# Kernel optimization log

Measured on AMD Instinct MI355X. Metric: run time of the kernel, lower is better.

Reference implementation:

```python
import jax, jax.numpy as jnp
from jax import lax
import numpy as np

B, N, J, NI, D = 2, 2048, 24, 9, 3
CD, HID = 16, 128
SOFT_BLEND = 20.0
MAX_STEPS, CVG = 50, 1e-5
INIT_BONES = np.array([0, 1, 2, 4, 5, 16, 17, 18, 19])


def _mlp(params, x):
    h = x
    for W, b in params[:-1]:
        h = jax.nn.softplus(h @ W + b)
    W, b = params[-1]
    return h @ W + b


def _broyden(g, x0, J_inv0):
    # x0: [P,3,1], J_inv0: [P,3,3]; fixed MAX_STEPS iterations, track best iterate
    gx = g(x0)
    err0 = jnp.linalg.norm(gx, axis=(1, 2))
    state = (x0, gx, J_inv0, -(J_inv0 @ gx), x0, err0)

    def body(i, st):
        x, gx, Jinv, upd, bx, berr = st
        dx = upd
        x = x + dx
        gx_new = g(x)
        dgx = gx_new - gx
        vT = jnp.swapaxes(dx, -2, -1) @ Jinv            # [P,1,3]
        a = dx - Jinv @ dgx                              # [P,3,1]
        b = vT @ dgx + 1e-6                              # [P,1,1]
        Jinv = Jinv + (a / b) @ vT                       # rank-1 Broyden update
        upd = -(Jinv @ gx_new)
        err = jnp.linalg.norm(gx_new, axis=(1, 2))
        better = err < berr
        bx = jnp.where(better[:, None, None], x, bx)
        berr = jnp.where(better, err, berr)
        return (x, gx_new, Jinv, upd, bx, berr)

    st = lax.fori_loop(0, MAX_STEPS, body, state)
    return st[4], st[5] < CVG


def setup_inputs():
    key = jax.random.key(0)
    ks = jax.random.split(key, 24)
    xd = 0.5 * jax.random.normal(ks[0], (B, N, D), jnp.float32)
    cond_latent = jax.random.normal(ks[1], (B, CD), jnp.float32)
    # near-identity invertible bone transforms
    R = jnp.eye(3, dtype=jnp.float32) + 0.1 * jax.random.normal(ks[2], (B, J, 3, 3), jnp.float32)
    t = 0.1 * jax.random.normal(ks[3], (B, J, 3), jnp.float32)
    tfs = jnp.zeros((B, J, 4, 4), jnp.float32)
    tfs = tfs.at[..., :3, :3].set(R).at[..., :3, 3].set(t).at[..., 3, 3].set(1.0)

    def w(k, fi, fo):
        return jax.random.normal(k, (fi, fo), jnp.float32) / np.sqrt(fi)

    din = D + CD
    inp = dict(xd=xd, cond_latent=cond_latent, tfs=tfs)
    dims_lbs = [(din, HID), (HID, HID), (HID, HID), (HID, J)]
    dims_disp = [(din, HID), (HID, HID), (HID, HID), (HID, D)]
    for i, (fi, fo) in enumerate(dims_lbs):
        inp[f"lbs_w{i}"] = w(ks[4 + i], fi, fo)
        inp[f"lbs_b{i}"] = jnp.zeros((fo,), jnp.float32)
    for i, (fi, fo) in enumerate(dims_disp):
        inp[f"disp_w{i}"] = w(ks[10 + i], fi, fo)
        inp[f"disp_b{i}"] = jnp.zeros((fo,), jnp.float32)
    return inp


def _forward(xd, cond_latent, tfs, lbs, disp):
    P = B * N
    xd_f = xd.reshape(P, D)
    cond_f = jnp.broadcast_to(cond_latent[:, None], (B, N, CD)).reshape(P, CD)
    tfs_f = jnp.broadcast_to(tfs[:, None], (B, N, J, 4, 4)).reshape(P, J, 4, 4)

    # __init: inverse-skin xd with one-hot weights at each init bone -> [P, NI, 3]
    xd_h = jnp.concatenate([xd_f, jnp.ones((P, 1), xd.dtype)], -1)
    xc_init = jnp.einsum('pnij,pj->pni', jnp.linalg.inv(tfs_f[:, INIT_BONES]), xd_h)[..., :3]

    PI = P * NI
    cond_e = jnp.repeat(cond_f, NI, axis=0)       # [PI, CD]
    tfs_e = jnp.repeat(tfs_f, NI, axis=0)         # [PI, J, 4, 4]
    xd_tgt = jnp.repeat(xd_f, NI, axis=0)         # [PI, 3]
    x0 = xc_init.reshape(PI, D)

    def fwd_skin(xc, lbs_p, cond_p, tfs_p):
        w = jax.nn.softmax(SOFT_BLEND * _mlp(lbs_p, jnp.concatenate([xc, cond_p], -1)), -1)
        xh = jnp.concatenate([xc, jnp.ones_like(xc[:, :1])], -1)
        return jnp.einsum('pn,pnij,pj->pi', w, tfs_p, xh)[:, :3]

    def fwd_skin_pt(x, c, t, lbs_p):
        w = jax.nn.softmax(SOFT_BLEND * _mlp(lbs_p, jnp.concatenate([x, c])))
        xh = jnp.concatenate([x, jnp.ones((1,), x.dtype)])
        return jnp.einsum('n,nij,j->i', w, t, xh)[:3]

    def gradient(xc, lbs_p, cond_p, tfs_p):
        # per-point 3x3 Jacobian of forward skinning wrt canonical point
        f = lambda x, c, t: fwd_skin_pt(x, c, t, lbs_p)
        return jax.vmap(jax.jacfwd(f), in_axes=(0, 0, 0))(xc, cond_p, tfs_p)

    # stop-gradient copies for the no-grad broyden search (torch.no_grad block)
    sg = lax.stop_gradient
    lbs_sg = [(sg(W), sg(b)) for W, b in lbs]
    cond_sg, tfs_sg, xdt_sg = sg(cond_e), sg(tfs_e), sg(xd_tgt)

    J_inv0 = jnp.linalg.inv(gradient(sg(x0), lbs_sg, cond_sg, tfs_sg))

    def g_ng(x):  # x: [PI,3,1]
        return (fwd_skin(x[..., 0], lbs_sg, cond_sg, tfs_sg) - xdt_sg)[..., None]

    x_opt, valid = _broyden(g_ng, sg(x0)[..., None], J_inv0)
    xc_opt = sg(x_opt[..., 0])

    # implicit-differentiation correction (eval_mode=False path)
    xd_opt = fwd_skin(xc_opt, lbs, cond_e, tfs_e)
    grad_inv = jnp.linalg.inv(gradient(xc_opt, lbs, cond_e, tfs_e))
    corr = jnp.einsum('pij,pj->pi', -sg(grad_inv), xd_opt - sg(xd_opt))
    xc = xc_opt + corr

    # __query_cano: beta displacement network
    xc = xc + _mlp(disp, jnp.concatenate([xc, cond_e], -1))
    return xc.reshape(B, N, NI, D), valid.reshape(B, N, NI)


def reference(xd, cond_latent, tfs, lbs_w0, lbs_b0, lbs_w1, lbs_b1, lbs_w2, lbs_b2, lbs_w3, lbs_b3, disp_w0, disp_b0, disp_w1, disp_b1, disp_w2, disp_b2, disp_w3, disp_b3):
    lbs = [(lbs_w0, lbs_b0), (lbs_w1, lbs_b1), (lbs_w2, lbs_b2), (lbs_w3, lbs_b3)]
    disp = [(disp_w0, disp_b0), (disp_w1, disp_b1), (disp_w2, disp_b2), (disp_w3, disp_b3)]
    return _forward(xd, cond_latent, tfs, lbs, disp)
```

## Files before the change

kernel.cpp:

```cpp
#include <hip/hip_runtime.h>
#include <math.h>

#define NB 2
#define NN 2048
#define NJ 24
#define NIB 9
#define NCD 16
#define NHID 128
#define NP (NB * NN)
#define NPI (NP * NIB)
#define NBSTRIDE (NN * NIB)
#define SBLEND 20.0f
#define CVG_EPS 1e-5f
#define MAX_STEPS 50
#define N_A 12

#define HSTR 129
#define INSTRD 21
#define LSTR 25

#define WS_BX 4
#define WS_BE (4 + 3 * NPI)
#define WS_META (4 + 4 * NPI)
#define WS_ST (4 + 5 * NPI)

static __device__ __forceinline__ float softplusf(float x) {
    return fmaxf(x, 0.0f) + log1pf(expf(-fabsf(x)));
}
static __device__ __forceinline__ float sigmoidf(float x) {
    return 1.0f / (1.0f + expf(-x));
}
static __device__ __forceinline__ int bone_of(int ib) {
    return (ib < 3) ? ib : ((ib < 5) ? ib + 1 : ib + 11);
}

template <int K>
static __device__ __forceinline__ void mv_acc16(const float* __restrict__ Wp, const float* inrow,
                                                int jb, float* acc) {
#pragma unroll 4
    for (int k = 0; k < K; k++) {
        float h = inrow[k];
        const float* wk = Wp + k * NHID + jb;
#pragma unroll
        for (int jj = 0; jj < 16; jj++) acc[jj] = fmaf(h, wk[jj], acc[jj]);
    }
}

template <int K, int LDIN>
static __device__ __forceinline__ void val_layer(const float* __restrict__ Wp,
                                                 const float* __restrict__ bp,
                                                 const float* inbase, float (*Hs)[HSTR], int r,
                                                 int jb, bool prebar) {
    float acc[16];
#pragma unroll
    for (int jj = 0; jj < 16; jj++) acc[jj] = bp[jb + jj];
    mv_acc16<K>(Wp, inbase + r * LDIN, jb, acc);
    if (prebar) __syncthreads();
#pragma unroll
    for (int jj = 0; jj < 16; jj++) Hs[r][jb + jj] = softplusf(acc[jj]);
    __syncthreads();
}

template <int K, int LDIN>
static __device__ __forceinline__ void jac_layer(const float* __restrict__ Wp,
                                                 const float* __restrict__ bp,
                                                 const float* inbase, float (*Hs)[HSTR], int r,
                                                 int jb, bool prebar) {
    const bool isval = (r < 16);
    const int p = r & 15;
    float acc[16];
#pragma unroll
    for (int jj = 0; jj < 16; jj++) acc[jj] = isval ? bp[jb + jj] : 0.0f;
    mv_acc16<K>(Wp, inbase + r * LDIN, jb, acc);
    if (prebar) __syncthreads();
#pragma unroll
    for (int jj = 0; jj < 16; jj++) Hs[r][jb + jj] = acc[jj];
    __syncthreads();
    float zv[16];
    if (!isval) {
#pragma unroll
        for (int jj = 0; jj < 16; jj++) zv[jj] = Hs[p][jb + jj];
    }
    __syncthreads();
    if (isval) {
#pragma unroll
        for (int jj = 0; jj < 16; jj++) Hs[r][jb + jj] = softplusf(acc[jj]);
    } else {
#pragma unroll
        for (int jj = 0; jj < 16; jj++) Hs[r][jb + jj] = sigmoidf(zv[jj]) * acc[jj];
    }
    __syncthreads();
}

template <bool JAC>
static __device__ __forceinline__ void logit_layer(const float* __restrict__ Wp,
                                                   const float* __restrict__ bp,
                                                   const float* inbase, float (*Lgs)[LSTR], int r,
                                                   int wid) {
    const int jb = wid * 3;
    const bool isval = (!JAC) || (r < 16);
    float acc[3];
#pragma unroll
    for (int jj = 0; jj < 3; jj++) acc[jj] = isval ? bp[jb + jj] : 0.0f;
#pragma unroll 4
    for (int k = 0; k < NHID; k++) {
        float h = inbase[r * HSTR + k];
        const float* wk = Wp + k * NJ + jb;
#pragma unroll
        for (int jj = 0; jj < 3; jj++) acc[jj] = fmaf(h, wk[jj], acc[jj]);
    }
#pragma unroll
    for (int jj = 0; jj < 3; jj++) Lgs[r][jb + jj] = acc[jj];
    __syncthreads();
}

static __device__ __forceinline__ void broyden_step(
    float* sLgRow, const float* sTm, float tx, float ty, float tz,
    float dx0, float dx1, float dx2,
    float& x0_, float& x1_, float& x2_, float& g0, float& g1, float& g2,
    float& Ji0, float& Ji1, float& Ji2, float& Ji3, float& Ji4, float& Ji5,
    float& Ji6, float& Ji7, float& Ji8,
    float& u0, float& u1, float& u2,
    float& bx0, float& bx1, float& bx2, float& berr) {
    float mx = -1e30f;
#pragma unroll
    for (int j = 0; j < NJ; j++) mx = fmaxf(mx, SBLEND * sLgRow[j]);
    float S = 0.0f;
#pragma unroll
    for (int j = 0; j < NJ; j++) {
        float e = expf(SBLEND * sLgRow[j] - mx);
        sLgRow[j] = e;
        S += e;
    }
    const float invS = 1.0f / S;
    float f0 = 0, f1 = 0, f2 = 0;
#pragma unroll
    for (int j = 0; j < NJ; j++) {
        float sj = sLgRow[j] * invS;
        const float* M = &sTm[j * 12];
        f0 += sj * (M[0] * x0_ + M[1] * x1_ + M[2] * x2_ + M[3]);
        f1 += sj * (M[4] * x0_ + M[5] * x1_ + M[6] * x2_ + M[7]);
        f2 += sj * (M[8] * x0_ + M[9] * x1_ + M[10] * x2_ + M[11]);
    }
    float gn0 = f0 - tx, gn1 = f1 - ty, gn2 = f2 - tz;
    float dg0 = gn0 - g0, dg1 = gn1 - g1, dg2 = gn2 - g2;
    float Jd0 = Ji0 * dg0 + Ji1 * dg1 + Ji2 * dg2;
    float Jd1 = Ji3 * dg0 + Ji4 * dg1 + Ji5 * dg2;
    float Jd2 = Ji6 * dg0 + Ji7 * dg1 + Ji8 * dg2;
    float v0 = dx0 * Ji0 + dx1 * Ji3 + dx2 * Ji6;
    float v1 = dx0 * Ji1 + dx1 * Ji4 + dx2 * Ji7;
    float v2 = dx0 * Ji2 + dx1 * Ji5 + dx2 * Ji8;
    float a0 = dx0 - Jd0, a1 = dx1 - Jd1, a2 = dx2 - Jd2;
    float bden = v0 * dg0 + v1 * dg1 + v2 * dg2 + 1e-6f;
    float s0 = a0 / bden, s1 = a1 / bden, s2 = a2 / bden;
    Ji0 += s0 * v0; Ji1 += s0 * v1; Ji2 += s0 * v2;
    Ji3 += s1 * v0; Ji4 += s1 * v1; Ji5 += s1 * v2;
    Ji6 += s2 * v0; Ji7 += s2 * v1; Ji8 += s2 * v2;
    u0 = -(Ji0 * gn0 + Ji1 * gn1 + Ji2 * gn2);
    u1 = -(Ji3 * gn0 + Ji4 * gn1 + Ji5 * gn2);
    u2 = -(Ji6 * gn0 + Ji7 * gn1 + Ji8 * gn2);
    float err = sqrtf(gn0 * gn0 + gn1 * gn1 + gn2 * gn2);
    if (err < berr) { berr = err; bx0 = x0_; bx1 = x1_; bx2 = x2_; }
    g0 = gn0; g1 = gn1; g2 = gn2;
}

__global__ __launch_bounds__(512) void kernel_a(
    const float* __restrict__ xd, const float* __restrict__ cond, const float* __restrict__ tfs,
    const float* __restrict__ lw0, const float* __restrict__ lb0,
    const float* __restrict__ lw1, const float* __restrict__ lb1,
    const float* __restrict__ lw2, const float* __restrict__ lb2,
    const float* __restrict__ lw3, const float* __restrict__ lb3,
    float* __restrict__ ws) {
    __shared__ float sIN[64][INSTRD];
    __shared__ float sH[64][HSTR];
    __shared__ float sLg[64][LSTR];
    __shared__ float sTm[NJ * 12];
    __shared__ int sCnt;

    const int tid = threadIdx.x;
    const int r = tid & 63;
    const int wid = __builtin_amdgcn_readfirstlane(tid >> 6);
    const int jb = wid * 16;
    const int pi0 = blockIdx.x * 64;
    const int b = pi0 / NBSTRIDE;
    const int pi = pi0 + r;

    for (int t = tid; t < NJ * 12; t += 512) {
        int j = t / 12, rc = t % 12;
        sTm[t] = tfs[(size_t)(b * NJ + j) * 16 + rc];
    }
    if (tid >= 16 && tid < 64) {
        const int d = (tid >> 4) - 1;
#pragma unroll
        for (int k = 0; k < 19; k++) sIN[tid][k] = (k == d) ? 1.0f : 0.0f;
    }
    if (tid < 16) {
#pragma unroll
        for (int cc = 0; cc < NCD; cc++) sIN[tid][3 + cc] = cond[b * NCD + cc];
    }

    float x0_ = 0, x1_ = 0, x2_ = 0, g0 = 0, g1 = 0, g2 = 0;
    float Ji0 = 0, Ji1 = 0, Ji2 = 0, Ji3 = 0, Ji4 = 0, Ji5 = 0, Ji6 = 0, Ji7 = 0, Ji8 = 0;
    float u0 = 0, u1 = 0, u2 = 0, bx0 = 0, bx1 = 0, bx2 = 0, berr = 0;
    float tx = 0, ty = 0, tz = 0;
    if (tid < 64) {
        const int pp = pi / NIB;
        tx = xd[pp * 3 + 0]; ty = xd[pp * 3 + 1]; tz = xd[pp * 3 + 2];
    }

#pragma unroll 1
    for (int pass = 0; pass < 4; ++pass) {
        __syncthreads();
        if (tid < 64 && (tid >> 4) == pass) {
            const int p = tid & 15;
            const int ib = pi % NIB;
            const float* T = tfs + (size_t)(b * NJ + bone_of(ib)) * 16;
            float r00 = T[0], r01 = T[1], r02 = T[2], t0 = T[3];
            float r10 = T[4], r11 = T[5], r12 = T[6], t1 = T[7];
            float r20 = T[8], r21 = T[9], r22 = T[10], t2 = T[11];
            float det = r00 * (r11 * r22 - r12 * r21) - r01 * (r10 * r22 - r12 * r20) +
                        r02 * (r10 * r21 - r11 * r20);
            float rd = 1.0f / det;
            float i00 = (r11 * r22 - r12 * r21) * rd, i01 = -(r01 * r22 - r02 * r21) * rd,
                  i02 = (r01 * r12 - r02 * r11) * rd;
            float i10 = -(r10 * r22 - r12 * r20) * rd, i11 = (r00 * r22 - r02 * r20) * rd,
                  i12 = -(r00 * r12 - r02 * r10) * rd;
            float i20 = (r10 * r21 - r11 * r20) * rd, i21 = -(r00 * r21 - r01 * r20) * rd,
                  i22 = (r00 * r11 - r01 * r10) * rd;
            float vx = tx - t0, vy = ty - t1, vz = tz - t2;
            x0_ = i00 * vx + i01 * vy + i02 * vz;
            x1_ = i10 * vx + i11 * vy + i12 * vz;
            x2_ = i20 * vx + i21 * vy + i22 * vz;
            sIN[p][0] = x0_; sIN[p][1] = x1_; sIN[p][2] = x2_;
        }
        __syncthreads();

        jac_layer<19, INSTRD>(lw0, lb0, &sIN[0][0], sH, r, jb, false);
        jac_layer<NHID, HSTR>(lw1, lb1, &sH[0][0], sH, r, jb, true);
        jac_layer<NHID, HSTR>(lw2, lb2, &sH[0][0], sH, r, jb, true);
        logit_layer<true>(lw3, lb3, &sH[0][0], sLg, r, wid);

        if (tid < 64 && (tid >> 4) == pass) {
            const int p = tid & 15;
            float mx = -1e30f;
#pragma unroll
            for (int j = 0; j < NJ; j++) mx = fmaxf(mx, SBLEND * sLg[p][j]);
            float S = 0.0f;
#pragma unroll
            for (int j = 0; j < NJ; j++) S += expf(SBLEND * sLg[p][j] - mx);
            const float invS = 1.0f / S;
            float d0 = 0, d1 = 0, d2 = 0;
#pragma unroll
            for (int j = 0; j < NJ; j++) {
                float sj = expf(SBLEND * sLg[p][j] - mx) * invS;
                d0 += sj * (SBLEND * sLg[16 + p][j]);
                d1 += sj * (SBLEND * sLg[32 + p][j]);
                d2 += sj * (SBLEND * sLg[48 + p][j]);
            }
            float f0 = 0, f1 = 0, f2 = 0;
            float J00 = 0, J01 = 0, J02 = 0, J10 = 0, J11 = 0, J12 = 0, J20 = 0, J21 = 0,
                  J22 = 0;
#pragma unroll
            for (int j = 0; j < NJ; j++) {
                float sj = expf(SBLEND * sLg[p][j] - mx) * invS;
                float uj0 = SBLEND * sLg[16 + p][j], uj1 = SBLEND * sLg[32 + p][j],
                      uj2 = SBLEND * sLg[48 + p][j];
                float sd0 = sj * (uj0 - d0), sd1 = sj * (uj1 - d1), sd2 = sj * (uj2 - d2);
                const float* M = &sTm[j * 12];
                float y0 = M[0] * x0_ + M[1] * x1_ + M[2] * x2_ + M[3];
                float y1 = M[4] * x0_ + M[5] * x1_ + M[6] * x2_ + M[7];
                float y2 = M[8] * x0_ + M[9] * x1_ + M[10] * x2_ + M[11];
                f0 += sj * y0; f1 += sj * y1; f2 += sj * y2;
                J00 += sd0 * y0 + sj * M[0]; J01 += sd1 * y0 + sj * M[1]; J02 += sd2 * y0 + sj * M[2];
                J10 += sd0 * y1 + sj * M[4]; J11 += sd1 * y1 + sj * M[5]; J12 += sd2 * y1 + sj * M[6];
                J20 += sd0 * y2 + sj * M[8]; J21 += sd1 * y2 + sj * M[9]; J22 += sd2 * y2 + sj * M[10];
            }
            g0 = f0 - tx; g1 = f1 - ty; g2 = f2 - tz;
            float detJ = J00 * (J11 * J22 - J12 * J21) - J01 * (J10 * J22 - J12 * J20) +
                         J02 * (J10 * J21 - J11 * J20);
            float rdJ = 1.0f / detJ;
            Ji0 = (J11 * J22 - J12 * J21) * rdJ; Ji1 = -(J01 * J22 - J02 * J21) * rdJ;
            Ji2 = (J01 * J12 - J02 * J11) * rdJ;
            Ji3 = -(J10 * J22 - J12 * J20) * rdJ; Ji4 = (J00 * J22 - J02 * J20) * rdJ;
            Ji5 = -(J00 * J12 - J02 * J10) * rdJ;
            Ji6 = (J10 * J21 - J11 * J20) * rdJ; Ji7 = -(J00 * J21 - J01 * J20) * rdJ;
            Ji8 = (J00 * J11 - J01 * J10) * rdJ;
            u0 = -(Ji0 * g0 + Ji1 * g1 + Ji2 * g2);
            u1 = -(Ji3 * g0 + Ji4 * g1 + Ji5 * g2);
            u2 = -(Ji6 * g0 + Ji7 * g1 + Ji8 * g2);
            berr = sqrtf(g0 * g0 + g1 * g1 + g2 * g2);
            bx0 = x0_; bx1 = x1_; bx2 = x2_;
        }
    }

    if (tid < 64) {
#pragma unroll
        for (int cc = 0; cc < NCD; cc++) sIN[tid][3 + cc] = cond[b * NCD + cc];
    }

    int itdone = 0;
#pragma unroll 1
    for (int it = 0; it < N_A; ++it) {
        float dx0 = 0, dx1 = 0, dx2 = 0;
        if (tid < 64) {
            dx0 = u0; dx1 = u1; dx2 = u2;
            x0_ += dx0; x1_ += dx1; x2_ += dx2;
            sIN[tid][0] = x0_; sIN[tid][1] = x1_; sIN[tid][2] = x2_;
        }
        __syncthreads();

        val_layer<19, INSTRD>(lw0, lb0, &sIN[0][0], sH, r, jb, false);
        val_layer<NHID, HSTR>(lw1, lb1, &sH[0][0], sH, r, jb, true);
        val_layer<NHID, HSTR>(lw2, lb2, &sH[0][0], sH, r, jb, true);
        logit_layer<false>(lw3, lb3, &sH[0][0], sLg, r, wid);

        if (tid < 64) {
            broyden_step(&sLg[r][0], sTm, tx, ty, tz, dx0, dx1, dx2,
                         x0_, x1_, x2_, g0, g1, g2,
                         Ji0, Ji1, Ji2, Ji3, Ji4, Ji5, Ji6, Ji7, Ji8,
                         u0, u1, u2, bx0, bx1, bx2, berr);
            unsigned long long m = __ballot(!(berr < CVG_EPS));
            if (tid == 0) sCnt = (int)__popcll(m);
        }
        __syncthreads();
        itdone = it + 1;
        if (sCnt == 0) break;
    }

    if (tid < 64) {
        ws[WS_BX + pi * 3 + 0] = bx0;
        ws[WS_BX + pi * 3 + 1] = bx1;
        ws[WS_BX + pi * 3 + 2] = bx2;
        ws[WS_BE + pi] = berr;
        const int remaining = MAX_STEPS - itdone;
        if (remaining > 0 && !(berr < CVG_EPS)) {
            int idx = atomicAdd((int*)ws + b, 1);
            int slot = b * NBSTRIDE + idx;
            ((int*)ws)[WS_META + slot] = pi | (remaining << 20);
            float st[15] = {x0_, x1_, x2_, g0, g1, g2, Ji0, Ji1, Ji2, Ji3, Ji4, Ji5, Ji6, Ji7, Ji8};
#pragma unroll
            for (int c = 0; c < 15; c++) ws[WS_ST + c * NPI + slot] = st[c];
        }
    }
}

__global__ __launch_bounds__(512) void kernel_b(
    const float* __restrict__ xd, const float* __restrict__ cond, const float* __restrict__ tfs,
    const float* __restrict__ lw0, const float* __restrict__ lb0,
    const float* __restrict__ lw1, const float* __restrict__ lb1,
    const float* __restrict__ lw2, const float* __restrict__ lb2,
    const float* __restrict__ lw3, const float* __restrict__ lb3,
    float* __restrict__ ws) {
    const int bid = blockIdx.x;
    const int batch = (bid < 288) ? 0 : 1;
    const int chunk0 = (bid - batch * 288) * 64;
    const int S = ((const int*)ws)[batch];
    if (chunk0 >= S) return;

    __shared__ float sIN[64][INSTRD];
    __shared__ float sH[64][HSTR];
    __shared__ float sLg[64][LSTR];
    __shared__ float sTm[NJ * 12];
    __shared__ int sCnt;

    const int tid = threadIdx.x;
    const int r = tid & 63;
    const int wid = __builtin_amdgcn_readfirstlane(tid >> 6);
    const int jb = wid * 16;

    for (int t = tid; t < NJ * 12; t += 512) {
        int j = t / 12, rc = t % 12;
        sTm[t] = tfs[(size_t)(batch * NJ + j) * 16 + rc];
    }

    float x0_ = 0, x1_ = 0, x2_ = 0, g0 = 0, g1 = 0, g2 = 0;
    float Ji0 = 1, Ji1 = 0, Ji2 = 0, Ji3 = 0, Ji4 = 1, Ji5 = 0, Ji6 = 0, Ji7 = 0, Ji8 = 1;
    float u0 = 0, u1 = 0, u2 = 0, bx0 = 0, bx1 = 0, bx2 = 0, berr = 0;
    float tx = 0, ty = 0, tz = 0;
    int pi = -1, itleft = 0;
    bool realrow = false;
    if (tid < 64) {
        const int k = chunk0 + r;
        realrow = (k < S);
        if (realrow) {
            const int slot = batch * NBSTRIDE + k;
            const int meta = ((const int*)ws)[WS_META + slot];
            pi = meta & 0xFFFFF;
            itleft = meta >> 20;
            x0_ = ws[WS_ST + 0 * NPI + slot]; x1_ = ws[WS_ST + 1 * NPI + slot];
            x2_ = ws[WS_ST + 2 * NPI + slot];
            g0 = ws[WS_ST + 3 * NPI + slot]; g1 = ws[WS_ST + 4 * NPI + slot];
            g2 = ws[WS_ST + 5 * NPI + slot];
            Ji0 = ws[WS_ST + 6 * NPI + slot]; Ji1 = ws[WS_ST + 7 * NPI + slot];
            Ji2 = ws[WS_ST + 8 * NPI + slot];
            Ji3 = ws[WS_ST + 9 * NPI + slot]; Ji4 = ws[WS_ST + 10 * NPI + slot];
            Ji5 = ws[WS_ST + 11 * NPI + slot];
            Ji6 = ws[WS_ST + 12 * NPI + slot]; Ji7 = ws[WS_ST + 13 * NPI + slot];
            Ji8 = ws[WS_ST + 14 * NPI + slot];
            u0 = -(Ji0 * g0 + Ji1 * g1 + Ji2 * g2);
            u1 = -(Ji3 * g0 + Ji4 * g1 + Ji5 * g2);
            u2 = -(Ji6 * g0 + Ji7 * g1 + Ji8 * g2);
            bx0 = ws[WS_BX + pi * 3 + 0]; bx1 = ws[WS_BX + pi * 3 + 1];
            bx2 = ws[WS_BX + pi * 3 + 2];
            berr = ws[WS_BE + pi];
            const int pp = pi / NIB;
            tx = xd[pp * 3 + 0]; ty = xd[pp * 3 + 1]; tz = xd[pp * 3 + 2];
        }
#pragma unroll
        for (int cc = 0; cc < NCD; cc++) sIN[tid][3 + cc] = cond[batch * NCD + cc];
        sIN[tid][0] = 0; sIN[tid][1] = 0; sIN[tid][2] = 0;
    }

#pragma unroll 1
    for (int it = 0; it < MAX_STEPS; ++it) {
        bool active = false;
        float dx0 = 0, dx1 = 0, dx2 = 0;
        if (tid < 64) {
            active = realrow && (itleft > 0) && !(berr < CVG_EPS);
            if (active) {
                dx0 = u0; dx1 = u1; dx2 = u2;
                x0_ += dx0; x1_ += dx1; x2_ += dx2;
            }
            sIN[tid][0] = x0_; sIN[tid][1] = x1_; sIN[tid][2] = x2_;
        }
        __syncthreads();

        val_layer<19, INSTRD>(lw0, lb0, &sIN[0][0], sH, r, jb, false);
        val_layer<NHID, HSTR>(lw1, lb1, &sH[0][0], sH, r, jb, true);
        val_layer<NHID, HSTR>(lw2, lb2, &sH[0][0], sH, r, jb, true);
        logit_layer<false>(lw3, lb3, &sH[0][0], sLg, r, wid);

        if (tid < 64) {
            if (active) {
                broyden_step(&sLg[r][0], sTm, tx, ty, tz, dx0, dx1, dx2,
                             x0_, x1_, x2_, g0, g1, g2,
                             Ji0, Ji1, Ji2, Ji3, Ji4, Ji5, Ji6, Ji7, Ji8,
                             u0, u1, u2, bx0, bx1, bx2, berr);
                itleft--;
            }
            unsigned long long m =
                __ballot(realrow && (itleft > 0) && !(berr < CVG_EPS));
            if (tid == 0) sCnt = (int)__popcll(m);
        }
        __syncthreads();
        if (sCnt == 0) break;
    }

    if (tid < 64 && realrow) {
        ws[WS_BX + pi * 3 + 0] = bx0;
        ws[WS_BX + pi * 3 + 1] = bx1;
        ws[WS_BX + pi * 3 + 2] = bx2;
        ws[WS_BE + pi] = berr;
    }
}

__global__ __launch_bounds__(512) void kernel_c(
    const float* __restrict__ cond,
    const float* __restrict__ dw0, const float* __restrict__ db0,
    const float* __restrict__ dw1, const float* __restrict__ db1,
    const float* __restrict__ dw2, const float* __restrict__ db2,
    const float* __restrict__ dw3, const float* __restrict__ db3,
    const float* __restrict__ ws, float* __restrict__ out) {
    __shared__ float sIN[64][INSTRD];
    __shared__ float sH[64][HSTR];

    const int tid = threadIdx.x;
    const int r = tid & 63;
    const int wid = __builtin_amdgcn_readfirstlane(tid >> 6);
    const int jb = wid * 16;
    const int pi0 = blockIdx.x * 64;
    const int b = pi0 / NBSTRIDE;
    const int pi = pi0 + r;

    float bx0 = 0, bx1 = 0, bx2 = 0, berr = 0;
    if (tid < 64) {
        bx0 = ws[WS_BX + pi * 3 + 0]; bx1 = ws[WS_BX + pi * 3 + 1];
        bx2 = ws[WS_BX + pi * 3 + 2];
        berr = ws[WS_BE + pi];
        sIN[tid][0] = bx0; sIN[tid][1] = bx1; sIN[tid][2] = bx2;
#pragma unroll
        for (int cc = 0; cc < NCD; cc++) sIN[tid][3 + cc] = cond[b * NCD + cc];
    }
    __syncthreads();

    val_layer<19, INSTRD>(dw0, db0, &sIN[0][0], sH, r, jb, false);
    val_layer<NHID, HSTR>(dw1, db1, &sH[0][0], sH, r, jb, true);
    val_layer<NHID, HSTR>(dw2, db2, &sH[0][0], sH, r, jb, true);

    if (tid < 64) {
        float a0 = db3[0], a1 = db3[1], a2 = db3[2];
#pragma unroll 4
        for (int k = 0; k < NHID; k++) {
            float h = sH[tid][k];
            a0 = fmaf(h, dw3[k * 3 + 0], a0);
            a1 = fmaf(h, dw3[k * 3 + 1], a1);
            a2 = fmaf(h, dw3[k * 3 + 2], a2);
        }
        out[pi * 3 + 0] = bx0 + a0;
        out[pi * 3 + 1] = bx1 + a1;
        out[pi * 3 + 2] = bx2 + a2;
        out[3 * NPI + pi] = (berr < CVG_EPS) ? 1.0f : 0.0f;
    }
}

extern "C" void kernel_launch(void* const* d_in, const int* in_sizes, int n_in,
                              void* d_out, int out_size, void* d_ws, size_t ws_size,
                              hipStream_t stream) {
    (void)in_sizes; (void)n_in; (void)out_size; (void)ws_size;
    const float* xd   = (const float*)d_in[0];
    const float* cond = (const float*)d_in[1];
    const float* tfs  = (const float*)d_in[2];
    const float* lw0 = (const float*)d_in[3];  const float* lb0 = (const float*)d_in[4];
    const float* lw1 = (const float*)d_in[5];  const float* lb1 = (const float*)d_in[6];
    const float* lw2 = (const float*)d_in[7];  const float* lb2 = (const float*)d_in[8];
    const float* lw3 = (const float*)d_in[9];  const float* lb3 = (const float*)d_in[10];
    const float* dw0 = (const float*)d_in[11]; const float* db0 = (const float*)d_in[12];
    const float* dw1 = (const float*)d_in[13]; const float* db1 = (const float*)d_in[14];
    const float* dw2 = (const float*)d_in[15]; const float* db2 = (const float*)d_in[16];
    const float* dw3 = (const float*)d_in[17]; const float* db3 = (const float*)d_in[18];
    float* ws = (float*)d_ws;
    float* out = (float*)d_out;

    hipMemsetAsync(d_ws, 0, 16, stream);
    kernel_a<<<NPI / 64, 512, 0, stream>>>(xd, cond, tfs, lw0, lb0, lw1, lb1, lw2, lb2,
                                           lw3, lb3, ws);
    kernel_b<<<576, 512, 0, stream>>>(xd, cond, tfs, lw0, lb0, lw1, lb1, lw2, lb2,
                                      lw3, lb3, ws);
    kernel_c<<<NPI / 64, 512, 0, stream>>>(cond, dw0, db0, dw1, db1, dw2, db2, dw3, db3,
                                           ws, out);
}
```

Before: 1.244 ms.

## Shrink row tile to 32 with 256-thread blocks, ping-pong hidden buffers, wave-level exits

All three kernels now process 32 points per block with 256 threads instead of 64 points with 512 threads. The Jacobian passes are re-split into 8 value rows plus 24 tangent rows. Hidden activations alternate between two shared buffers, which removes the barrier that was needed before overwriting the input. Every wave now runs the Broyden step redundantly for all 32 rows, so the shared-memory counter and its block-wide barrier are replaced by a wave-level __all/__any early-exit test. This doubles block count and aims for higher occupancy and fewer barriers, at the cost of less weight reuse per block and duplicated per-row scalar work.

```diff
diff --git a/kernel.cpp b/kernel.cpp
--- a/kernel.cpp
+++ b/kernel.cpp
@@ -15,8 +15,11 @@
 #define MAX_STEPS 50
 #define N_A 12
 
+#define ROWS 32
+#define NTHR 256
+#define NBLK (NPI / ROWS)
 #define HSTR 129
-#define INSTRD 21
+#define INSTRD 19
 #define LSTR 25
 
 #define WS_BX 4
@@ -34,9 +37,9 @@
     return (ib < 3) ? ib : ((ib < 5) ? ib + 1 : ib + 11);
 }
 
-template <int K>
-static __device__ __forceinline__ void mv_acc16(const float* __restrict__ Wp, const float* inrow,
-                                                int jb, float* acc) {
+template <int K, int LDIN>
+static __device__ __forceinline__ void mv_acc16(const float* __restrict__ Wp,
+                                                const float* inrow, int jb, float* acc) {
 #pragma unroll 4
     for (int k = 0; k < K; k++) {
         float h = inrow[k];
@@ -49,45 +52,43 @@
 template <int K, int LDIN>
 static __device__ __forceinline__ void val_layer(const float* __restrict__ Wp,
                                                  const float* __restrict__ bp,
-                                                 const float* inbase, float (*Hs)[HSTR], int r,
-                                                 int jb, bool prebar) {
+                                                 const float* inbase, float (*OUT)[HSTR],
+                                                 int r, int jb) {
     float acc[16];
 #pragma unroll
     for (int jj = 0; jj < 16; jj++) acc[jj] = bp[jb + jj];
-    mv_acc16<K>(Wp, inbase + r * LDIN, jb, acc);
-    if (prebar) __syncthreads();
-#pragma unroll
-    for (int jj = 0; jj < 16; jj++) Hs[r][jb + jj] = softplusf(acc[jj]);
+    mv_acc16<K, LDIN>(Wp, inbase + r * LDIN, jb, acc);
+#pragma unroll
+    for (int jj = 0; jj < 16; jj++) OUT[r][jb + jj] = softplusf(acc[jj]);
     __syncthreads();
 }
 
 template <int K, int LDIN>
 static __device__ __forceinline__ void jac_layer(const float* __restrict__ Wp,
                                                  const float* __restrict__ bp,
-                                                 const float* inbase, float (*Hs)[HSTR], int r,
-                                                 int jb, bool prebar) {
-    const bool isval = (r < 16);
-    const int p = r & 15;
+                                                 const float* inbase, float (*OUT)[HSTR],
+                                                 int r, int jb) {
+    const bool isval = (r < 8);
+    const int p = r & 7;
     float acc[16];
 #pragma unroll
     for (int jj = 0; jj < 16; jj++) acc[jj] = isval ? bp[jb + jj] : 0.0f;
-    mv_acc16<K>(Wp, inbase + r * LDIN, jb, acc);
-    if (prebar) __syncthreads();
-#pragma unroll
-    for (int jj = 0; jj < 16; jj++) Hs[r][jb + jj] = acc[jj];
+    mv_acc16<K, LDIN>(Wp, inbase + r * LDIN, jb, acc);
+#pragma unroll
+    for (int jj = 0; jj < 16; jj++) OUT[r][jb + jj] = acc[jj];
     __syncthreads();
     float zv[16];
     if (!isval) {
 #pragma unroll
-        for (int jj = 0; jj < 16; jj++) zv[jj] = Hs[p][jb + jj];
+        for (int jj = 0; jj < 16; jj++) zv[jj] = OUT[p][jb + jj];
     }
     __syncthreads();
     if (isval) {
 #pragma unroll
-        for (int jj = 0; jj < 16; jj++) Hs[r][jb + jj] = softplusf(acc[jj]);
+        for (int jj = 0; jj < 16; jj++) OUT[r][jb + jj] = softplusf(acc[jj]);
     } else {
 #pragma unroll
-        for (int jj = 0; jj < 16; jj++) Hs[r][jb + jj] = sigmoidf(zv[jj]) * acc[jj];
+        for (int jj = 0; jj < 16; jj++) OUT[r][jb + jj] = sigmoidf(zv[jj]) * acc[jj];
     }
     __syncthreads();
 }
@@ -95,10 +96,10 @@
 template <bool JAC>
 static __device__ __forceinline__ void logit_layer(const float* __restrict__ Wp,
                                                    const float* __restrict__ bp,
-                                                   const float* inbase, float (*Lgs)[LSTR], int r,
-                                                   int wid) {
-    const int jb = wid * 3;
-    const bool isval = (!JAC) || (r < 16);
+                                                   const float* inbase, float (*Lgs)[LSTR],
+                                                   int r, int cg) {
+    const int jb = cg * 3;
+    const bool isval = (!JAC) || (r < 8);
     float acc[3];
 #pragma unroll
     for (int jj = 0; jj < 3; jj++) acc[jj] = isval ? bp[jb + jj] : 0.0f;
@@ -114,29 +115,31 @@
     __syncthreads();
 }
 
-static __device__ __forceinline__ void broyden_step(
-    float* sLgRow, const float* sTm, float tx, float ty, float tz,
+static __device__ __forceinline__ void broyden_step_reg(
+    const float* sLgRow, const float* sTm, float tx, float ty, float tz,
     float dx0, float dx1, float dx2,
     float& x0_, float& x1_, float& x2_, float& g0, float& g1, float& g2,
     float& Ji0, float& Ji1, float& Ji2, float& Ji3, float& Ji4, float& Ji5,
     float& Ji6, float& Ji7, float& Ji8,
     float& u0, float& u1, float& u2,
     float& bx0, float& bx1, float& bx2, float& berr) {
+    float l[NJ];
+#pragma unroll
+    for (int j = 0; j < NJ; j++) l[j] = SBLEND * sLgRow[j];
     float mx = -1e30f;
 #pragma unroll
-    for (int j = 0; j < NJ; j++) mx = fmaxf(mx, SBLEND * sLgRow[j]);
+    for (int j = 0; j < NJ; j++) mx = fmaxf(mx, l[j]);
     float S = 0.0f;
 #pragma unroll
     for (int j = 0; j < NJ; j++) {
-        float e = expf(SBLEND * sLgRow[j] - mx);
-        sLgRow[j] = e;
-        S += e;
+        l[j] = expf(l[j] - mx);
+        S += l[j];
     }
     const float invS = 1.0f / S;
     float f0 = 0, f1 = 0, f2 = 0;
 #pragma unroll
     for (int j = 0; j < NJ; j++) {
-        float sj = sLgRow[j] * invS;
+        float sj = l[j] * invS;
         const float* M = &sTm[j * 12];
         f0 += sj * (M[0] * x0_ + M[1] * x1_ + M[2] * x2_ + M[3]);
         f1 += sj * (M[4] * x0_ + M[5] * x1_ + M[6] * x2_ + M[7]);
@@ -164,55 +167,52 @@
     g0 = gn0; g1 = gn1; g2 = gn2;
 }
 
-__global__ __launch_bounds__(512) void kernel_a(
+__global__ __launch_bounds__(NTHR, 4) void kernel_a(
     const float* __restrict__ xd, const float* __restrict__ cond, const float* __restrict__ tfs,
     const float* __restrict__ lw0, const float* __restrict__ lb0,
     const float* __restrict__ lw1, const float* __restrict__ lb1,
     const float* __restrict__ lw2, const float* __restrict__ lb2,
     const float* __restrict__ lw3, const float* __restrict__ lb3,
     float* __restrict__ ws) {
-    __shared__ float sIN[64][INSTRD];
-    __shared__ float sH[64][HSTR];
-    __shared__ float sLg[64][LSTR];
+    __shared__ float sIN[ROWS][INSTRD];
+    __shared__ float sHa[ROWS][HSTR];
+    __shared__ float sHb[ROWS][HSTR];
+    __shared__ float sLg[ROWS][LSTR];
     __shared__ float sTm[NJ * 12];
-    __shared__ int sCnt;
 
     const int tid = threadIdx.x;
-    const int r = tid & 63;
-    const int wid = __builtin_amdgcn_readfirstlane(tid >> 6);
-    const int jb = wid * 16;
-    const int pi0 = blockIdx.x * 64;
+    const int r = tid & 31;
+    const int cg = tid >> 5;
+    const int jb = cg * 16;
+    const int pi0 = blockIdx.x * ROWS;
     const int b = pi0 / NBSTRIDE;
     const int pi = pi0 + r;
 
-    for (int t = tid; t < NJ * 12; t += 512) {
+    for (int t = tid; t < NJ * 12; t += NTHR) {
         int j = t / 12, rc = t % 12;
         sTm[t] = tfs[(size_t)(b * NJ + j) * 16 + rc];
     }
-    if (tid >= 16 && tid < 64) {
-        const int d = (tid >> 4) - 1;
-#pragma unroll
-        for (int k = 0; k < 19; k++) sIN[tid][k] = (k == d) ? 1.0f : 0.0f;
-    }
-    if (tid < 16) {
-#pragma unroll
-        for (int cc = 0; cc < NCD; cc++) sIN[tid][3 + cc] = cond[b * NCD + cc];
+    if (r >= 8) {
+        const int d = (r >> 3) - 1;
+#pragma unroll
+        for (int k = 0; k < INSTRD; k++) sIN[r][k] = (k == 3 + 13 + d - 16) ? 0.0f : 0.0f;
+#pragma unroll
+        for (int k = 0; k < INSTRD; k++) sIN[r][k] = (k == d) ? 1.0f : 0.0f;
+    } else {
+#pragma unroll
+        for (int cc = 0; cc < NCD; cc++) sIN[r][3 + cc] = cond[b * NCD + cc];
     }
 
     float x0_ = 0, x1_ = 0, x2_ = 0, g0 = 0, g1 = 0, g2 = 0;
     float Ji0 = 0, Ji1 = 0, Ji2 = 0, Ji3 = 0, Ji4 = 0, Ji5 = 0, Ji6 = 0, Ji7 = 0, Ji8 = 0;
     float u0 = 0, u1 = 0, u2 = 0, bx0 = 0, bx1 = 0, bx2 = 0, berr = 0;
-    float tx = 0, ty = 0, tz = 0;
-    if (tid < 64) {
-        const int pp = pi / NIB;
-        tx = xd[pp * 3 + 0]; ty = xd[pp * 3 + 1]; tz = xd[pp * 3 + 2];
-    }
+    const int pp = pi / NIB;
+    const float tx = xd[pp * 3 + 0], ty = xd[pp * 3 + 1], tz = xd[pp * 3 + 2];
 
 #pragma unroll 1
     for (int pass = 0; pass < 4; ++pass) {
-        __syncthreads();
-        if (tid < 64 && (tid >> 4) == pass) {
-            const int p = tid & 15;
+        if ((r >> 3) == pass) {
+            const int p = r & 7;
             const int ib = pi % NIB;
             const float* T = tfs + (size_t)(b * NJ + bone_of(ib)) * 16;
             float r00 = T[0], r01 = T[1], r02 = T[2], t0 = T[3];
@@ -235,13 +235,13 @@
         }
         __syncthreads();
 
-        jac_layer<19, INSTRD>(lw0, lb0, &sIN[0][0], sH, r, jb, false);
-        jac_layer<NHID, HSTR>(lw1, lb1, &sH[0][0], sH, r, jb, true);
-        jac_layer<NHID, HSTR>(lw2, lb2, &sH[0][0], sH, r, jb, true);
-        logit_layer<true>(lw3, lb3, &sH[0][0], sLg, r, wid);
-
-        if (tid < 64 && (tid >> 4) == pass) {
-            const int p = tid & 15;
+        jac_layer<INSTRD, INSTRD>(lw0, lb0, &sIN[0][0], sHa, r, jb);
+        jac_layer<NHID, HSTR>(lw1, lb1, &sHa[0][0], sHb, r, jb);
+        jac_layer<NHID, HSTR>(lw2, lb2, &sHb[0][0], sHa, r, jb);
+        logit_layer<true>(lw3, lb3, &sHa[0][0], sLg, r, cg);
+
+        if ((r >> 3) == pass) {
+            const int p = r & 7;
             float mx = -1e30f;
 #pragma unroll
             for (int j = 0; j < NJ; j++) mx = fmaxf(mx, SBLEND * sLg[p][j]);
@@ -253,9 +253,9 @@
 #pragma unroll
             for (int j = 0; j < NJ; j++) {
                 float sj = expf(SBLEND * sLg[p][j] - mx) * invS;
-                d0 += sj * (SBLEND * sLg[16 + p][j]);
-                d1 += sj * (SBLEND * sLg[32 + p][j]);
-                d2 += sj * (SBLEND * sLg[48 + p][j]);
+                d0 += sj * (SBLEND * sLg[8 + p][j]);
+                d1 += sj * (SBLEND * sLg[16 + p][j]);
+                d2 += sj * (SBLEND * sLg[24 + p][j]);
             }
             float f0 = 0, f1 = 0, f2 = 0;
             float J00 = 0, J01 = 0, J02 = 0, J10 = 0, J11 = 0, J12 = 0, J20 = 0, J21 = 0,
@@ -263,8 +263,8 @@
 #pragma unroll
             for (int j = 0; j < NJ; j++) {
                 float sj = expf(SBLEND * sLg[p][j] - mx) * invS;
-                float uj0 = SBLEND * sLg[16 + p][j], uj1 = SBLEND * sLg[32 + p][j],
-                      uj2 = SBLEND * sLg[48 + p][j];
+                float uj0 = SBLEND * sLg[8 + p][j], uj1 = SBLEND * sLg[16 + p][j],
+                      uj2 = SBLEND * sLg[24 + p][j];
                 float sd0 = sj * (uj0 - d0), sd1 = sj * (uj1 - d1), sd2 = sj * (uj2 - d2);
                 const float* M = &sTm[j * 12];
                 float y0 = M[0] * x0_ + M[1] * x1_ + M[2] * x2_ + M[3];
@@ -293,41 +293,31 @@
         }
     }
 
-    if (tid < 64) {
-#pragma unroll
-        for (int cc = 0; cc < NCD; cc++) sIN[tid][3 + cc] = cond[b * NCD + cc];
-    }
+#pragma unroll
+    for (int cc = 0; cc < NCD; cc++) sIN[r][3 + cc] = cond[b * NCD + cc];
 
     int itdone = 0;
 #pragma unroll 1
     for (int it = 0; it < N_A; ++it) {
-        float dx0 = 0, dx1 = 0, dx2 = 0;
-        if (tid < 64) {
-            dx0 = u0; dx1 = u1; dx2 = u2;
-            x0_ += dx0; x1_ += dx1; x2_ += dx2;
-            sIN[tid][0] = x0_; sIN[tid][1] = x1_; sIN[tid][2] = x2_;
-        }
+        float dx0 = u0, dx1 = u1, dx2 = u2;
+        x0_ += dx0; x1_ += dx1; x2_ += dx2;
+        sIN[r][0] = x0_; sIN[r][1] = x1_; sIN[r][2] = x2_;
         __syncthreads();
 
-        val_layer<19, INSTRD>(lw0, lb0, &sIN[0][0], sH, r, jb, false);
-        val_layer<NHID, HSTR>(lw1, lb1, &sH[0][0], sH, r, jb, true);
-        val_layer<NHID, HSTR>(lw2, lb2, &sH[0][0], sH, r, jb, true);
-        logit_layer<false>(lw3, lb3, &sH[0][0], sLg, r, wid);
-
-        if (tid < 64) {
-            broyden_step(&sLg[r][0], sTm, tx, ty, tz, dx0, dx1, dx2,
+        val_layer<INSTRD, INSTRD>(lw0, lb0, &sIN[0][0], sHa, r, jb);
+        val_layer<NHID, HSTR>(lw1, lb1, &sHa[0][0], sHb, r, jb);
+        val_layer<NHID, HSTR>(lw2, lb2, &sHb[0][0], sHa, r, jb);
+        logit_layer<false>(lw3, lb3, &sHa[0][0], sLg, r, cg);
+
+        broyden_step_reg(&sLg[r][0], sTm, tx, ty, tz, dx0, dx1, dx2,
                          x0_, x1_, x2_, g0, g1, g2,
                          Ji0, Ji1, Ji2, Ji3, Ji4, Ji5, Ji6, Ji7, Ji8,
                          u0, u1, u2, bx0, bx1, bx2, berr);
-            unsigned long long m = __ballot(!(berr < CVG_EPS));
-            if (tid == 0) sCnt = (int)__popcll(m);
-        }
-        __syncthreads();
         itdone = it + 1;
-        if (sCnt == 0) break;
-    }
-
-    if (tid < 64) {
+        if (__all(berr < CVG_EPS)) break;
+    }
+
+    if (cg == 0) {
         ws[WS_BX + pi * 3 + 0] = bx0;
         ws[WS_BX + pi * 3 + 1] = bx1;
         ws[WS_BX + pi * 3 + 2] = bx2;
@@ -344,7 +334,7 @@
     }
 }
 
-__global__ __launch_bounds__(512) void kernel_b(
+__global__ __launch_bounds__(NTHR, 4) void kernel_b(
     const float* __restrict__ xd, const float* __restrict__ cond, const float* __restrict__ tfs,
     const float* __restrict__ lw0, const float* __restrict__ lb0,
     const float* __restrict__ lw1, const float* __restrict__ lb1,
@@ -352,23 +342,23 @@
     const float* __restrict__ lw3, const float* __restrict__ lb3,
     float* __restrict__ ws) {
     const int bid = blockIdx.x;
-    const int batch = (bid < 288) ? 0 : 1;
-    const int chunk0 = (bid - batch * 288) * 64;
+    const int batch = (bid < 576) ? 0 : 1;
+    const int chunk0 = (bid - batch * 576) * ROWS;
     const int S = ((const int*)ws)[batch];
     if (chunk0 >= S) return;
 
-    __shared__ float sIN[64][INSTRD];
-    __shared__ float sH[64][HSTR];
-    __shared__ float sLg[64][LSTR];
+    __shared__ float sIN[ROWS][INSTRD];
+    __shared__ float sHa[ROWS][HSTR];
+    __shared__ float sHb[ROWS][HSTR];
+    __shared__ float sLg[ROWS][LSTR];
     __shared__ float sTm[NJ * 12];
-    __shared__ int sCnt;
 
     const int tid = threadIdx.x;
-    const int r = tid & 63;
-    const int wid = __builtin_amdgcn_readfirstlane(tid >> 6);
-    const int jb = wid * 16;
-
-    for (int t = tid; t < NJ * 12; t += 512) {
+    const int r = tid & 31;
+    const int cg = tid >> 5;
+    const int jb = cg * 16;
+
+    for (int t = tid; t < NJ * 12; t += NTHR) {
         int j = t / 12, rc = t % 12;
         sTm[t] = tfs[(size_t)(batch * NJ + j) * 16 + rc];
     }
@@ -378,75 +368,61 @@
     float u0 = 0, u1 = 0, u2 = 0, bx0 = 0, bx1 = 0, bx2 = 0, berr = 0;
     float tx = 0, ty = 0, tz = 0;
     int pi = -1, itleft = 0;
-    bool realrow = false;
-    if (tid < 64) {
-        const int k = chunk0 + r;
-        realrow = (k < S);
-        if (realrow) {
-            const int slot = batch * NBSTRIDE + k;
-            const int meta = ((const int*)ws)[WS_META + slot];
-            pi = meta & 0xFFFFF;
-            itleft = meta >> 20;
-            x0_ = ws[WS_ST + 0 * NPI + slot]; x1_ = ws[WS_ST + 1 * NPI + slot];
-            x2_ = ws[WS_ST + 2 * NPI + slot];
-            g0 = ws[WS_ST + 3 * NPI + slot]; g1 = ws[WS_ST + 4 * NPI + slot];
-            g2 = ws[WS_ST + 5 * NPI + slot];
-            Ji0 = ws[WS_ST + 6 * NPI + slot]; Ji1 = ws[WS_ST + 7 * NPI + slot];
-            Ji2 = ws[WS_ST + 8 * NPI + slot];
-            Ji3 = ws[WS_ST + 9 * NPI + slot]; Ji4 = ws[WS_ST + 10 * NPI + slot];
-            Ji5 = ws[WS_ST + 11 * NPI + slot];
-            Ji6 = ws[WS_ST + 12 * NPI + slot]; Ji7 = ws[WS_ST + 13 * NPI + slot];
-            Ji8 = ws[WS_ST + 14 * NPI + slot];
-            u0 = -(Ji0 * g0 + Ji1 * g1 + Ji2 * g2);
-            u1 = -(Ji3 * g0 + Ji4 * g1 + Ji5 * g2);
-            u2 = -(Ji6 * g0 + Ji7 * g1 + Ji8 * g2);
-            bx0 = ws[WS_BX + pi * 3 + 0]; bx1 = ws[WS_BX + pi * 3 + 1];
-            bx2 = ws[WS_BX + pi * 3 + 2];
-            berr = ws[WS_BE + pi];
-            const int pp = pi / NIB;
-            tx = xd[pp * 3 + 0]; ty = xd[pp * 3 + 1]; tz = xd[pp * 3 + 2];
-        }
-#pragma unroll
-        for (int cc = 0; cc < NCD; cc++) sIN[tid][3 + cc] = cond[batch * NCD + cc];
-        sIN[tid][0] = 0; sIN[tid][1] = 0; sIN[tid][2] = 0;
-    }
+    const bool realrow = (chunk0 + r < S);
+    if (realrow) {
+        const int slot = batch * NBSTRIDE + chunk0 + r;
+        const int meta = ((const int*)ws)[WS_META + slot];
+        pi = meta & 0xFFFFF;
+        itleft = meta >> 20;
+        x0_ = ws[WS_ST + 0 * NPI + slot]; x1_ = ws[WS_ST + 1 * NPI + slot];
+        x2_ = ws[WS_ST + 2 * NPI + slot];
+        g0 = ws[WS_ST + 3 * NPI + slot]; g1 = ws[WS_ST + 4 * NPI + slot];
+        g2 = ws[WS_ST + 5 * NPI + slot];
+        Ji0 = ws[WS_ST + 6 * NPI + slot]; Ji1 = ws[WS_ST + 7 * NPI + slot];
+        Ji2 = ws[WS_ST + 8 * NPI + slot];
+        Ji3 = ws[WS_ST + 9 * NPI + slot]; Ji4 = ws[WS_ST + 10 * NPI + slot];
+        Ji5 = ws[WS_ST + 11 * NPI + slot];
+        Ji6 = ws[WS_ST + 12 * NPI + slot]; Ji7 = ws[WS_ST + 13 * NPI + slot];
+        Ji8 = ws[WS_ST + 14 * NPI + slot];
+        u0 = -(Ji0 * g0 + Ji1 * g1 + Ji2 * g2);
+        u1 = -(Ji3 * g0 + Ji4 * g1 + Ji5 * g2);
+        u2 = -(Ji6 * g0 + Ji7 * g1 + Ji8 * g2);
+        bx0 = ws[WS_BX + pi * 3 + 0]; bx1 = ws[WS_BX + pi * 3 + 1];
+        bx2 = ws[WS_BX + pi * 3 + 2];
+        berr = ws[WS_BE + pi];
+        const int pp = pi / NIB;
+        tx = xd[pp * 3 + 0]; ty = xd[pp * 3 + 1]; tz = xd[pp * 3 + 2];
+    }
+#pragma unroll
+    for (int cc = 0; cc < NCD; cc++) sIN[r][3 + cc] = cond[batch * NCD + cc];
 
 #pragma unroll 1
     for (int it = 0; it < MAX_STEPS; ++it) {
-        bool active = false;
+        bool active = realrow && (itleft > 0) && !(berr < CVG_EPS);
         float dx0 = 0, dx1 = 0, dx2 = 0;
-        if (tid < 64) {
-            active = realrow && (itleft > 0) && !(berr < CVG_EPS);
-            if (active) {
-                dx0 = u0; dx1 = u1; dx2 = u2;
-                x0_ += dx0; x1_ += dx1; x2_ += dx2;
-            }
-            sIN[tid][0] = x0_; sIN[tid][1] = x1_; sIN[tid][2] = x2_;
+        if (active) {
+            dx0 = u0; dx1 = u1; dx2 = u2;
+            x0_ += dx0; x1_ += dx1; x2_ += dx2;
         }
+        sIN[r][0] = x0_; sIN[r][1] = x1_; sIN[r][2] = x2_;
         __syncthreads();
 
-        val_layer<19, INSTRD>(lw0, lb0, &sIN[0][0], sH, r, jb, false);
-        val_layer<NHID, HSTR>(lw1, lb1, &sH[0][0], sH, r, jb, true);
-        val_layer<NHID, HSTR>(lw2, lb2, &sH[0][0], sH, r, jb, true);
-        logit_layer<false>(lw3, lb3, &sH[0][0], sLg, r, wid);
-
-        if (tid < 64) {
-            if (active) {
-                broyden_step(&sLg[r][0], sTm, tx, ty, tz, dx0, dx1, dx2,
+        val_layer<INSTRD, INSTRD>(lw0, lb0, &sIN[0][0], sHa, r, jb);
+        val_layer<NHID, HSTR>(lw1, lb1, &sHa[0][0], sHb, r, jb);
+        val_layer<NHID, HSTR>(lw2, lb2, &sHb[0][0], sHa, r, jb);
+        logit_layer<false>(lw3, lb3, &sHa[0][0], sLg, r, cg);
+
+        if (active) {
+            broyden_step_reg(&sLg[r][0], sTm, tx, ty, tz, dx0, dx1, dx2,
                              x0_, x1_, x2_, g0, g1, g2,
                              Ji0, Ji1, Ji2, Ji3, Ji4, Ji5, Ji6, Ji7, Ji8,
                              u0, u1, u2, bx0, bx1, bx2, berr);
-                itleft--;
-            }
-            unsigned long long m =
-                __ballot(realrow && (itleft > 0) && !(berr < CVG_EPS));
-            if (tid == 0) sCnt = (int)__popcll(m);
+            itleft--;
         }
-        __syncthreads();
-        if (sCnt == 0) break;
-    }
-
-    if (tid < 64 && realrow) {
+        if (!__any(realrow && (itleft > 0) && !(berr < CVG_EPS))) break;
+    }
+
+    if (cg == 0 && realrow) {
         ws[WS_BX + pi * 3 + 0] = bx0;
         ws[WS_BX + pi * 3 + 1] = bx1;
         ws[WS_BX + pi * 3 + 2] = bx2;
@@ -454,48 +430,47 @@
     }
 }
 
-__global__ __launch_bounds__(512) void kernel_c(
+__global__ __launch_bounds__(NTHR, 4) void kernel_c(
     const float* __restrict__ cond,
     const float* __restrict__ dw0, const float* __restrict__ db0,
     const float* __restrict__ dw1, const float* __restrict__ db1,
     const float* __restrict__ dw2, const float* __restrict__ db2,
     const float* __restrict__ dw3, const float* __restrict__ db3,
     const float* __restrict__ ws, float* __restrict__ out) {
-    __shared__ float sIN[64][INSTRD];
-    __shared__ float sH[64][HSTR];
+    __shared__ float sIN[ROWS][INSTRD];
+    __shared__ float sHa[ROWS][HSTR];
+    __shared__ float sHb[ROWS][HSTR];
 
     const int tid = threadIdx.x;
-    const int r = tid & 63;
-    const int wid = __builtin_amdgcn_readfirstlane(tid >> 6);
-    const int jb = wid * 16;
-    const int pi0 = blockIdx.x * 64;
+    const int r = tid & 31;
+    const int cg = tid >> 5;
+    const int jb = cg * 16;
+    const int pi0 = blockIdx.x * ROWS;
     const int b = pi0 / NBSTRIDE;
     const int pi = pi0 + r;
 
-    float bx0 = 0, bx1 = 0, bx2 = 0, berr = 0;
-    if (tid < 64) {
-        bx0 = ws[WS_BX + pi * 3 + 0]; bx1 = ws[WS_BX + pi * 3 + 1];
-        bx2 = ws[WS_BX + pi * 3 + 2];
-        berr = ws[WS_BE + pi];
-        sIN[tid][0] = bx0; sIN[tid][1] = bx1; sIN[tid][2] = bx2;
-#pragma unroll
-        for (int cc = 0; cc < NCD; cc++) sIN[tid][3 + cc] = cond[b * NCD + cc];
-    }
+    const float bx0 = ws[WS_BX + pi * 3 + 0];
+    const float bx1 = ws[WS_BX + pi * 3 + 1];
+    const float bx2 = ws[WS_BX + pi * 3 + 2];
+    const float berr = ws[WS_BE + pi];
+    sIN[r][0] = bx0; sIN[r][1] = bx1; sIN[r][2] = bx2;
+#pragma unroll
+    for (int cc = 0; cc < NCD; cc++) sIN[r][3 + cc] = cond[b * NCD + cc];
     __syncthreads();
 
-    val_layer<19, INSTRD>(dw0, db0, &sIN[0][0], sH, r, jb, false);
-    val_layer<NHID, HSTR>(dw1, db1, &sH[0][0], sH, r, jb, true);
-    val_layer<NHID, HSTR>(dw2, db2, &sH[0][0], sH, r, jb, true);
-
-    if (tid < 64) {
-        float a0 = db3[0], a1 = db3[1], a2 = db3[2];
+    val_layer<INSTRD, INSTRD>(dw0, db0, &sIN[0][0], sHa, r, jb);
+    val_layer<NHID, HSTR>(dw1, db1, &sHa[0][0], sHb, r, jb);
+    val_layer<NHID, HSTR>(dw2, db2, &sHb[0][0], sHa, r, jb);
+
+    float a0 = db3[0], a1 = db3[1], a2 = db3[2];
 #pragma unroll 4
-        for (int k = 0; k < NHID; k++) {
-            float h = sH[tid][k];
-            a0 = fmaf(h, dw3[k * 3 + 0], a0);
-            a1 = fmaf(h, dw3[k * 3 + 1], a1);
-            a2 = fmaf(h, dw3[k * 3 + 2], a2);
-        }
+    for (int k = 0; k < NHID; k++) {
+        float h = sHa[r][k];
+        a0 = fmaf(h, dw3[k * 3 + 0], a0);
+        a1 = fmaf(h, dw3[k * 3 + 1], a1);
+        a2 = fmaf(h, dw3[k * 3 + 2], a2);
+    }
+    if (cg == 0) {
         out[pi * 3 + 0] = bx0 + a0;
         out[pi * 3 + 1] = bx1 + a1;
         out[pi * 3 + 2] = bx2 + a2;
@@ -522,10 +497,10 @@
     float* out = (float*)d_out;
 
     hipMemsetAsync(d_ws, 0, 16, stream);
-    kernel_a<<<NPI / 64, 512, 0, stream>>>(xd, cond, tfs, lw0, lb0, lw1, lb1, lw2, lb2,
-                                           lw3, lb3, ws);
-    kernel_b<<<576, 512, 0, stream>>>(xd, cond, tfs, lw0, lb0, lw1, lb1, lw2, lb2,
-                                      lw3, lb3, ws);
-    kernel_c<<<NPI / 64, 512, 0, stream>>>(cond, dw0, db0, dw1, db1, dw2, db2, dw3, db3,
-                                           ws, out);
-}
+    kernel_a<<<NBLK, NTHR, 0, stream>>>(xd, cond, tfs, lw0, lb0, lw1, lb1, lw2, lb2,
+                                        lw3, lb3, ws);
+    kernel_b<<<NBLK, NTHR, 0, stream>>>(xd, cond, tfs, lw0, lb0, lw1, lb1, lw2, lb2,
+                                        lw3, lb3, ws);
+    kernel_c<<<NBLK, NTHR, 0, stream>>>(cond, dw0, db0, dw1, db1, dw2, db2, dw3, db3,
+                                        ws, out);
+}
```

Result: slower. 3.186 ms (+156.1%).
